# Optimization experiments

Hardware: AMD Instinct MI355X
Metric: run time of the kernel (lower is better)

## Reference

```python
import jax, jax.numpy as jnp
import numpy as np

B, T, D, HS = 8, 2048, 1024, 64


def setup_inputs() -> dict:
    key = jax.random.key(0)
    ks = jax.random.split(key, 7)
    return {
        "x": jax.random.normal(ks[0], (B, T, D), dtype=jnp.float32),
        "Wq": jax.random.normal(ks[1], (D, HS), dtype=jnp.float32) / np.sqrt(D),
        "bq": jax.random.normal(ks[2], (HS,), dtype=jnp.float32) * 0.01,
        "Wk": jax.random.normal(ks[3], (D, HS), dtype=jnp.float32) / np.sqrt(D),
        "bk": jax.random.normal(ks[4], (HS,), dtype=jnp.float32) * 0.01,
        "Wv": jax.random.normal(ks[5], (D, HS), dtype=jnp.float32) / np.sqrt(D),
        "bv": jax.random.normal(ks[6], (HS,), dtype=jnp.float32) * 0.01,
    }


def reference(x, Wq, bq, Wk, bk, Wv, bv):
    # Q,K,V projections: [B,T,D] @ [D,HS] -> [B,T,HS]
    Q = x @ Wq + bq
    K = x @ Wk + bk
    V = x @ Wv + bv
    # raw scores [B,T,T]
    scores = jnp.einsum("bqh,bkh->bqk", Q, K)
    # causal mask applied BEFORE scaling (as in the original; -inf is scale-invariant)
    causal = jnp.tril(jnp.ones((T, T), dtype=bool))
    scores = jnp.where(causal[None, :, :], scores, -jnp.inf)
    scores = scores / jnp.sqrt(jnp.asarray(HS, dtype=scores.dtype))
    attn = jax.nn.softmax(scores, axis=-1)
    # dropout is identity in eval mode (deterministic reference)
    return jnp.einsum("bqk,bkh->bqh", attn, V)
```

## Files before the change

kernel.cpp:

```cpp
#include <hip/hip_runtime.h>
#include <hip/hip_bf16.h>

typedef __bf16 bf16x8 __attribute__((ext_vector_type(8)));
typedef __bf16 bf16x4 __attribute__((ext_vector_type(4)));
typedef float  f32x4  __attribute__((ext_vector_type(4)));

#define B_  8
#define T_  2048
#define D_  1024
#define HS_ 64


__global__ __launch_bounds__(256) void pack_w(
    const float* __restrict__ Wq, const float* __restrict__ Wk,
    const float* __restrict__ Wv, __bf16* __restrict__ Wp)
{
    const int t    = blockIdx.x * 256 + threadIdx.x;
    const int lane = t & 63;
    const int pg   = t >> 6;
    const int s    = pg & 3;
    const int c    = (pg >> 2) & 31;
    const int p    = pg >> 7;
    const int m16  = lane & 15;
    const int quad = lane >> 4;

    const float* W = (p == 0) ? Wq : (p == 1) ? Wk : Wv;
    const float* src = W + (size_t)(c * 32 + quad * 8) * 64 + s * 16 + m16;
    bf16x8 frag;
    #pragma unroll
    for (int j = 0; j < 8; ++j) frag[j] = (__bf16)src[(size_t)j * 64];
    *(bf16x8*)(Wp + (size_t)pg * 512 + lane * 8) = frag;
}

__global__ __launch_bounds__(256) void qkv_fused(
    const float* __restrict__ x,
    const __bf16* __restrict__ Wp,
    const float* __restrict__ bq, const float* __restrict__ bk,
    const float* __restrict__ bv,
    __bf16* __restrict__ Q,
    __bf16* __restrict__ Kp,
    __bf16* __restrict__ Vp)
{
    __shared__ alignas(16) unsigned char Smem[73728];

    const int rt   = blockIdx.x;
    const int wave = threadIdx.x >> 6;
    const int lane = threadIdx.x & 63;
    const int m16  = lane & 15;
    const int quad = lane >> 4;
    const int row0 = rt * 32;

    __bf16* Xs = (__bf16*)(Smem + wave * 16896);

    {
        const float* xsrc = x + (size_t)row0 * 1024 + wave * 256;
        const int sr = lane >> 5;
        const int sc = (lane & 31) * 8;
        #pragma unroll
        for (int i = 0; i < 16; ++i) {
            const int r = i * 2 + sr;
            f32x4 v0 = *(const f32x4*)(xsrc + (size_t)r * 1024 + sc);
            f32x4 v1 = *(const f32x4*)(xsrc + (size_t)r * 1024 + sc + 4);
            bf16x8 w;
            #pragma unroll
            for (int e = 0; e < 4; ++e) { w[e] = (__bf16)v0[e]; w[4 + e] = (__bf16)v1[e]; }
            *(bf16x8*)&Xs[r * 264 + sc] = w;
        }
    }
    __builtin_amdgcn_wave_barrier();

    f32x4 acc[3][4][2];
    #pragma unroll
    for (int p = 0; p < 3; ++p)
        #pragma unroll
        for (int s = 0; s < 4; ++s)
            #pragma unroll
            for (int t = 0; t < 2; ++t) acc[p][s][t] = {0.f, 0.f, 0.f, 0.f};

    bf16x8 bfA[12], bfB[12];

#define WLOAD(BUF, K0)                                                     \
    {                                                                      \
        const int cb_ = wave * 8 + ((K0) >> 5);                            \
        _Pragma("unroll")                                                  \
        for (int ps_ = 0; ps_ < 12; ++ps_) {                               \
            const int p_ = ps_ >> 2, s_ = ps_ & 3;                         \
            BUF[ps_] = *(const bf16x8*)(Wp +                               \
                ((size_t)((p_ * 32 + cb_) * 4 + s_) << 9) + lane * 8);     \
        }                                                                  \
    }
#define KSTEP(BUF, K0)                                                     \
    {                                                                      \
        bf16x8 a0 = *(const bf16x8*)&Xs[m16 * 264 + (K0) + quad * 8];      \
        bf16x8 a1 = *(const bf16x8*)&Xs[(16 + m16) * 264 + (K0) + quad * 8]; \
        __builtin_amdgcn_sched_barrier(0);                                 \
        _Pragma("unroll")                                                  \
        for (int ps_ = 0; ps_ < 12; ++ps_) {                               \
            acc[ps_ >> 2][ps_ & 3][0] =                                    \
                __builtin_amdgcn_mfma_f32_16x16x32_bf16(a0, BUF[ps_], acc[ps_ >> 2][ps_ & 3][0], 0, 0, 0); \
            acc[ps_ >> 2][ps_ & 3][1] =                                    \
                __builtin_amdgcn_mfma_f32_16x16x32_bf16(a1, BUF[ps_], acc[ps_ >> 2][ps_ & 3][1], 0, 0, 0); \
        }                                                                  \
    }

    WLOAD(bfA, 0);
    #pragma unroll
    for (int k0 = 0; k0 < 256; k0 += 64) {
        WLOAD(bfB, k0 + 32);
        KSTEP(bfA, k0);
        if (k0 + 64 < 256) WLOAD(bfA, k0 + 64);
        KSTEP(bfB, k0 + 32);
    }
#undef KSTEP
#undef WLOAD

    f32x4* Red = (f32x4*)Smem;
    __syncthreads();
    if (wave != 0) {
        #pragma unroll
        for (int p = 0; p < 3; ++p)
            #pragma unroll
            for (int s = 0; s < 4; ++s)
                #pragma unroll
                for (int t = 0; t < 2; ++t)
                    Red[((wave - 1) * 24 + (p * 4 + s) * 2 + t) * 64 + lane] = acc[p][s][t];
    }
    __syncthreads();
    if (wave != 0) return;

    #pragma unroll
    for (int p = 0; p < 3; ++p)
        #pragma unroll
        for (int s = 0; s < 4; ++s)
            #pragma unroll
            for (int t = 0; t < 2; ++t) {
                f32x4 sum = acc[p][s][t];
                #pragma unroll
                for (int w = 0; w < 3; ++w) {
                    f32x4 v = Red[(w * 24 + (p * 4 + s) * 2 + t) * 64 + lane];
                    #pragma unroll
                    for (int e = 0; e < 4; ++e) sum[e] += v[e];
                }
                acc[p][s][t] = sum;
            }

    #pragma unroll
    for (int t = 0; t < 2; ++t) {
        const int row0t = row0 + t * 16;

        #pragma unroll
        for (int s = 0; s < 4; ++s) {
            const int h = s * 16 + m16;
            const float bia = bq[h];
            #pragma unroll
            for (int r = 0; r < 4; ++r)
                Q[(size_t)(row0t + quad * 4 + r) * 64 + h] = (__bf16)(acc[0][s][t][r] + bia);
        }

        const int tb = (row0t >> 4) & 3;
        const int jt = (row0t >> 6) & 31;
        const int bb = row0t >> 11;
        __bf16* kpt = Kp + (((size_t)bb * 32 + jt) * 8) * 512;
        __bf16* vpt = Vp + (((size_t)bb * 32 + jt) * 8) * 512;

        {
            const int snb  = ((tb >> 1) << 1) | (quad & 1);
            const int m16b = ((tb & 1) << 3) | ((quad >> 1) << 2);
            #pragma unroll
            for (int s = 0; s < 4; ++s) {
                const int h = s * 16 + m16;
                const float bia = bk[h];
                const int g     = snb * 2 + (s >> 1);
                const int quadc = ((s & 1) << 1) | (m16 >> 3);
                const int j     = m16 & 7;
                #pragma unroll
                for (int r = 0; r < 4; ++r)
                    kpt[(size_t)g * 512 + (quadc * 16 + m16b + r) * 8 + j] =
                        (__bf16)(acc[1][s][t][r] + bia);
            }
        }
        {
            const int lanec = ((((tb & 1) << 1) | (quad >> 1)) << 4) + m16;
            const int jbase = (quad & 1) << 2;
            #pragma unroll
            for (int s = 0; s < 4; ++s) {
                const int h = s * 16 + m16;
                const float bia = bv[h];
                const int g = s * 2 + (tb >> 1);
                bf16x4 pack;
                #pragma unroll
                for (int r = 0; r < 4; ++r) pack[r] = (__bf16)(acc[2][s][t][r] + bia);
                *(bf16x4*)(vpt + (size_t)g * 512 + lanec * 8 + jbase) = pack;
            }
        }
    }
}

__global__ __launch_bounds__(512) void attn_fused(
    const __bf16* __restrict__ Q,
    const __bf16* __restrict__ Kp,
    const __bf16* __restrict__ Vp,
    float* __restrict__ O)
{
    __shared__ float Mrg[8][64][37];

    const int s  = blockIdx.x;
    const int b  = blockIdx.y;
    const int wave = threadIdx.x >> 6;
    const int lane = threadIdx.x & 63;
    const int m16  = lane & 15;
    const int quad = lane >> 4;
    const float SC = 0.18033688f;

    const __bf16* Qb = Q  + (size_t)b * T_ * HS_;
    const __bf16* Kb = Kp + (size_t)b * 32 * 4096;
    const __bf16* Vb = Vp + (size_t)b * 32 * 4096;
    float* Obase     = O  + (size_t)b * T_ * HS_;

    bf16x8 vA[8];

#define LOADK(KA, JT)                                                      \
    {                                                                      \
        const __bf16* kb_ = Kb + (size_t)(JT) * 4096 + lane * 8;           \
        _Pragma("unroll")                                                  \
        for (int g_ = 0; g_ < 8; ++g_) KA[g_] = *(const bf16x8*)(kb_ + g_ * 512); \
    }
#define LOADV(JT)                                                          \
    {                                                                      \
        const __bf16* vb_ = Vb + (size_t)(JT) * 4096 + lane * 8;           \
        _Pragma("unroll")                                                  \
        for (int g_ = 0; g_ < 8; ++g_) vA[g_] = *(const bf16x8*)(vb_ + g_ * 512); \
    }

#define STEP(CK, NK)                                                       \
    {                                                                      \
        const int j0 = jt * 64;                                            \
        LOADV(jt);                       \
        f32x4 svA[4], svB[4];                                              \
        _Pragma("unroll")                                                  \
        for (int sn_ = 0; sn_ < 4; ++sn_) {                                \
            svA[sn_] = {0.f, 0.f, 0.f, 0.f};                               \
            svB[sn_] = {0.f, 0.f, 0.f, 0.f};                               \
            svA[sn_] = __builtin_amdgcn_mfma_f32_16x16x32_bf16(CK[sn_*2],   qA0, svA[sn_], 0, 0, 0); \
            svA[sn_] = __builtin_amdgcn_mfma_f32_16x16x32_bf16(CK[sn_*2+1], qA1, svA[sn_], 0, 0, 0); \
            svB[sn_] = __builtin_amdgcn_mfma_f32_16x16x32_bf16(CK[sn_*2],   qB0, svB[sn_], 0, 0, 0); \
            svB[sn_] = __builtin_amdgcn_mfma_f32_16x16x32_bf16(CK[sn_*2+1], qB1, svB[sn_], 0, 0, 0); \
        }                                                                  \
        if (jt + 8 < ntiles) LOADK(NK, jt + 8);                            \
        __builtin_amdgcn_sched_barrier(0);                                 \
        if (jt == ntiles - 1) {    \
            _Pragma("unroll")                                              \
            for (int sn_ = 0; sn_ < 4; ++sn_) {                            \
                const int kbase = j0 + ((sn_ >> 1) << 5) + (quad << 3) + ((sn_ & 1) << 2); \
                _Pragma("unroll")                                          \
                for (int r_ = 0; r_ < 4; ++r_) {                           \
                    svA[sn_][r_] = (kbase + r_ <= qrowA) ? svA[sn_][r_] : -3e38f; \
                    svB[sn_][r_] = (kbase + r_ <= qrowB) ? svB[sn_][r_] : -3e38f; \
                }                                                          \
            }                                                              \
        }                                                                  \
        float mxA = -3e38f, mxB = -3e38f;                                  \
        _Pragma("unroll")                                                  \
        for (int sn_ = 0; sn_ < 4; ++sn_)                                  \
            _Pragma("unroll")                                              \
            for (int r_ = 0; r_ < 4; ++r_) {                               \
                mxA = fmaxf(mxA, svA[sn_][r_]);                            \
                mxB = fmaxf(mxB, svB[sn_][r_]);                            \
            }                                                              \
        mxA = fmaxf(mxA, __shfl_xor(mxA, 16));                             \
        mxA = fmaxf(mxA, __shfl_xor(mxA, 32));                             \
        mxB = fmaxf(mxB, __shfl_xor(mxB, 16));                             \
        mxB = fmaxf(mxB, __shfl_xor(mxB, 32));                             \
        const float newmA = fmaxf(mA, mxA);                                \
        const float newmB = fmaxf(mB, mxB);                                \
        const float alA = exp2f((mA - newmA) * SC);                        \
        const float alB = exp2f((mB - newmB) * SC);                        \
        mA = newmA; mB = newmB;                                            \
        const float nmA = newmA * SC, nmB = newmB * SC;                    \
        float rsA = 0.f, rsB = 0.f;                                        \
        _Pragma("unroll")                                                  \
        for (int sn_ = 0; sn_ < 4; ++sn_)                                  \
            _Pragma("unroll")                                              \
            for (int r_ = 0; r_ < 4; ++r_) {                               \
                float pa_ = exp2f(__builtin_fmaf(svA[sn_][r_], SC, -nmA)); \
                float pb_ = exp2f(__builtin_fmaf(svB[sn_][r_], SC, -nmB)); \
                svA[sn_][r_] = pa_; rsA += pa_;                            \
                svB[sn_][r_] = pb_; rsB += pb_;                            \
            }                                                              \
        rsA += __shfl_xor(rsA, 16); rsA += __shfl_xor(rsA, 32);            \
        rsB += __shfl_xor(rsB, 16); rsB += __shfl_xor(rsB, 32);            \
        lA = lA * alA + rsA;  lB = lB * alB + rsB;                         \
        _Pragma("unroll")                                                  \
        for (int hs_ = 0; hs_ < 4; ++hs_)                                  \
            _Pragma("unroll")                                              \
            for (int r_ = 0; r_ < 4; ++r_) {                               \
                oA[hs_][r_] *= alA;                                        \
                oB[hs_][r_] *= alB;                                        \
            }                                                              \
        bf16x8 pA0, pA1, pB0, pB1;                                         \
        _Pragma("unroll")                                                  \
        for (int r_ = 0; r_ < 4; ++r_) {                                   \
            pA0[r_]     = (__bf16)svA[0][r_];                              \
            pA0[4 + r_] = (__bf16)svA[1][r_];                              \
            pA1[r_]     = (__bf16)svA[2][r_];                              \
            pA1[4 + r_] = (__bf16)svA[3][r_];                              \
            pB0[r_]     = (__bf16)svB[0][r_];                              \
            pB0[4 + r_] = (__bf16)svB[1][r_];                              \
            pB1[r_]     = (__bf16)svB[2][r_];                              \
            pB1[4 + r_] = (__bf16)svB[3][r_];                              \
        }                                                                  \
        _Pragma("unroll")                                                  \
        for (int hs_ = 0; hs_ < 4; ++hs_) {                                \
            oA[hs_] = __builtin_amdgcn_mfma_f32_16x16x32_bf16(vA[hs_*2],   pA0, oA[hs_], 0, 0, 0); \
            oA[hs_] = __builtin_amdgcn_mfma_f32_16x16x32_bf16(vA[hs_*2+1], pA1, oA[hs_], 0, 0, 0); \
            oB[hs_] = __builtin_amdgcn_mfma_f32_16x16x32_bf16(vA[hs_*2],   pB0, oB[hs_], 0, 0, 0); \
            oB[hs_] = __builtin_amdgcn_mfma_f32_16x16x32_bf16(vA[hs_*2+1], pB1, oB[hs_], 0, 0, 0); \
        }                                                                  \
    }

    auto runPhase = [&](const int f) {
        const int ntiles = (f >> 1) + 1;
        const int qrowA  = f * 32 + m16;
        const int qrowB  = qrowA + 16;

        bf16x8 qA0 = *(const bf16x8*)(Qb + (size_t)qrowA * 64 + quad * 8);
        bf16x8 qA1 = *(const bf16x8*)(Qb + (size_t)qrowA * 64 + 32 + quad * 8);
        bf16x8 qB0 = *(const bf16x8*)(Qb + (size_t)qrowB * 64 + quad * 8);
        bf16x8 qB1 = *(const bf16x8*)(Qb + (size_t)qrowB * 64 + 32 + quad * 8);

        f32x4 oA[4], oB[4];
        #pragma unroll
        for (int hs = 0; hs < 4; ++hs) {
            oA[hs] = {0.f, 0.f, 0.f, 0.f};
            oB[hs] = {0.f, 0.f, 0.f, 0.f};
        }
        float mA = -3e38f, lA = 0.f, mB = -3e38f, lB = 0.f;

        bf16x8 kA[8], kB[8];
        int jt = wave;
        if (jt < ntiles) {
            LOADK(kA, jt);
            while (true) {
                STEP(kA, kB);
                jt += 8; if (jt >= ntiles) break;
                STEP(kB, kA);
                jt += 8; if (jt >= ntiles) break;
            }
        }

        #pragma unroll
        for (int hs = 0; hs < 4; ++hs)
            #pragma unroll
            for (int r = 0; r < 4; ++r) {
                Mrg[wave][lane][hs * 4 + r]      = oA[hs][r];
                Mrg[wave][lane][18 + hs * 4 + r] = oB[hs][r];
            }
        Mrg[wave][lane][16] = mA; Mrg[wave][lane][17] = lA;
        Mrg[wave][lane][34] = mB; Mrg[wave][lane][35] = lB;
        __syncthreads();
        if (wave < 2) {
            const int off  = wave * 18;
            const int qrow = f * 32 + wave * 16 + m16;
            float mw[8], lw[8];
            #pragma unroll
            for (int w = 0; w < 8; ++w) {
                mw[w] = Mrg[w][lane][off + 16];
                lw[w] = Mrg[w][lane][off + 17];
            }
            float M = mw[0];
            #pragma unroll
            for (int w = 1; w < 8; ++w) M = fmaxf(M, mw[w]);
            float aw[8], den = 0.f;
            #pragma unroll
            for (int w = 0; w < 8; ++w) {
                aw[w] = exp2f((mw[w] - M) * SC);
                den += lw[w] * aw[w];
            }
            const float inv = 1.f / den;
            float* Ob = Obase + (size_t)qrow * 64;
            #pragma unroll
            for (int hs = 0; hs < 4; ++hs) {
                f32x4 v;
                #pragma unroll
                for (int r = 0; r < 4; ++r) {
                    float acc = 0.f;
                    #pragma unroll
                    for (int w = 0; w < 8; ++w)
                        acc += Mrg[w][lane][off + hs * 4 + r] * aw[w];
                    v[r] = acc * inv;
                }
                *(f32x4*)(Ob + hs * 16 + quad * 4) = v;
            }
        }
        __syncthreads();
    };

    runPhase(s);
    runPhase(63 - s);
#undef STEP
#undef LOADV
#undef LOADK
}

extern "C" void kernel_launch(void* const* d_in, const int* in_sizes, int n_in,
                              void* d_out, int out_size, void* d_ws, size_t ws_size,
                              hipStream_t stream)
{
    const float* x  = (const float*)d_in[0];
    const float* Wq = (const float*)d_in[1];
    const float* bq = (const float*)d_in[2];
    const float* Wk = (const float*)d_in[3];
    const float* bk = (const float*)d_in[4];
    const float* Wv = (const float*)d_in[5];
    const float* bv = (const float*)d_in[6];
    float* out = (float*)d_out;

    __bf16* Wp = (__bf16*)d_ws;
    __bf16* Q  = Wp + 384 * 512;
    __bf16* Kp = Q  + (size_t)B_ * T_ * HS_;
    __bf16* Vp = Kp + (size_t)B_ * T_ * HS_;

    pack_w<<<96, 256, 0, stream>>>(Wq, Wk, Wv, Wp);
    qkv_fused<<<512, 256, 0, stream>>>(x, Wp, bq, bk, bv, Q, Kp, Vp);
    attn_fused<<<dim3(32, 8), 512, 0, stream>>>(Q, Kp, Vp, out);
}
```

Baseline: 128.1 us.

## Split QKV projection across waves by output tile instead of K-reduction

The QKV projection kernel now processes 16 rows per block (1024 blocks) with a shared 16x1024 bf16 x tile. Each wave owns 3 of the 12 output column tiles and runs the full K=1024 reduction itself, rather than each wave covering a quarter of K and merging partials through LDS. This removes the cross-wave reduction, its LDS traffic and one barrier, shrinks LDS to about 33KB, and cuts accumulator registers so more blocks fit per CU (launch bounds now request 4). In exchange every block rereads the full packed weight matrix, doubling weight traffic from L2, and each wave has a longer serial MFMA chain with fewer independent accumulators.

```diff
diff --git a/kernel.cpp b/kernel.cpp
--- a/kernel.cpp
+++ b/kernel.cpp
@@ -32,7 +32,7 @@
     *(bf16x8*)(Wp + (size_t)pg * 512 + lane * 8) = frag;
 }
 
-__global__ __launch_bounds__(256) void qkv_fused(
+__global__ __launch_bounds__(256, 4) void qkv_fused(
     const float* __restrict__ x,
     const __bf16* __restrict__ Wp,
     const float* __restrict__ bq, const float* __restrict__ bk,
@@ -41,157 +41,109 @@
     __bf16* __restrict__ Kp,
     __bf16* __restrict__ Vp)
 {
-    __shared__ alignas(16) unsigned char Smem[73728];
+    __shared__ alignas(16) __bf16 Xs[16 * 1032];
 
     const int rt   = blockIdx.x;
     const int wave = threadIdx.x >> 6;
     const int lane = threadIdx.x & 63;
     const int m16  = lane & 15;
     const int quad = lane >> 4;
-    const int row0 = rt * 32;
-
-    __bf16* Xs = (__bf16*)(Smem + wave * 16896);
+    const int row0 = rt * 16;
 
     {
         const float* xsrc = x + (size_t)row0 * 1024 + wave * 256;
         const int sr = lane >> 5;
         const int sc = (lane & 31) * 8;
         #pragma unroll
-        for (int i = 0; i < 16; ++i) {
+        for (int i = 0; i < 8; ++i) {
             const int r = i * 2 + sr;
             f32x4 v0 = *(const f32x4*)(xsrc + (size_t)r * 1024 + sc);
             f32x4 v1 = *(const f32x4*)(xsrc + (size_t)r * 1024 + sc + 4);
             bf16x8 w;
             #pragma unroll
             for (int e = 0; e < 4; ++e) { w[e] = (__bf16)v0[e]; w[4 + e] = (__bf16)v1[e]; }
-            *(bf16x8*)&Xs[r * 264 + sc] = w;
-        }
-    }
-    __builtin_amdgcn_wave_barrier();
-
-    f32x4 acc[3][4][2];
-    #pragma unroll
-    for (int p = 0; p < 3; ++p)
-        #pragma unroll
-        for (int s = 0; s < 4; ++s)
-            #pragma unroll
-            for (int t = 0; t < 2; ++t) acc[p][s][t] = {0.f, 0.f, 0.f, 0.f};
-
-    bf16x8 bfA[12], bfB[12];
-
-#define WLOAD(BUF, K0)                                                     \
-    {                                                                      \
-        const int cb_ = wave * 8 + ((K0) >> 5);                            \
-        _Pragma("unroll")                                                  \
-        for (int ps_ = 0; ps_ < 12; ++ps_) {                               \
-            const int p_ = ps_ >> 2, s_ = ps_ & 3;                         \
-            BUF[ps_] = *(const bf16x8*)(Wp +                               \
-                ((size_t)((p_ * 32 + cb_) * 4 + s_) << 9) + lane * 8);     \
-        }                                                                  \
-    }
-#define KSTEP(BUF, K0)                                                     \
-    {                                                                      \
-        bf16x8 a0 = *(const bf16x8*)&Xs[m16 * 264 + (K0) + quad * 8];      \
-        bf16x8 a1 = *(const bf16x8*)&Xs[(16 + m16) * 264 + (K0) + quad * 8]; \
+            *(bf16x8*)&Xs[r * 1032 + wave * 256 + sc] = w;
+        }
+    }
+    __syncthreads();
+
+    const int ps0 = wave * 3;
+    const __bf16* wb[3];
+    #pragma unroll
+    for (int j = 0; j < 3; ++j) {
+        const int ps = ps0 + j, p = ps >> 2, s = ps & 3;
+        wb[j] = Wp + (size_t)p * 65536 + s * 512 + lane * 8;
+    }
+    const __bf16* ab = &Xs[m16 * 1032 + quad * 8];
+
+    f32x4 acc[3];
+    #pragma unroll
+    for (int j = 0; j < 3; ++j) acc[j] = {0.f, 0.f, 0.f, 0.f};
+
+    bf16x8 bfA[3], bfB[3];
+
+#define WLOAD(BUF, C)                                                      \
+    {                                                                      \
+        _Pragma("unroll")                                                  \
+        for (int j_ = 0; j_ < 3; ++j_)                                     \
+            BUF[j_] = *(const bf16x8*)(wb[j_] + (size_t)(C) * 2048);       \
+    }
+#define KSTEP(BUF, C)                                                      \
+    {                                                                      \
+        bf16x8 a_ = *(const bf16x8*)(ab + (C) * 32);                       \
         __builtin_amdgcn_sched_barrier(0);                                 \
         _Pragma("unroll")                                                  \
-        for (int ps_ = 0; ps_ < 12; ++ps_) {                               \
-            acc[ps_ >> 2][ps_ & 3][0] =                                    \
-                __builtin_amdgcn_mfma_f32_16x16x32_bf16(a0, BUF[ps_], acc[ps_ >> 2][ps_ & 3][0], 0, 0, 0); \
-            acc[ps_ >> 2][ps_ & 3][1] =                                    \
-                __builtin_amdgcn_mfma_f32_16x16x32_bf16(a1, BUF[ps_], acc[ps_ >> 2][ps_ & 3][1], 0, 0, 0); \
-        }                                                                  \
+        for (int j_ = 0; j_ < 3; ++j_)                                     \
+            acc[j_] = __builtin_amdgcn_mfma_f32_16x16x32_bf16(a_, BUF[j_], acc[j_], 0, 0, 0); \
     }
 
     WLOAD(bfA, 0);
-    #pragma unroll
-    for (int k0 = 0; k0 < 256; k0 += 64) {
-        WLOAD(bfB, k0 + 32);
-        KSTEP(bfA, k0);
-        if (k0 + 64 < 256) WLOAD(bfA, k0 + 64);
-        KSTEP(bfB, k0 + 32);
+    WLOAD(bfB, 1);
+    #pragma unroll
+    for (int c = 0; c < 32; c += 2) {
+        KSTEP(bfA, c);
+        if (c + 2 < 32) WLOAD(bfA, c + 2);
+        KSTEP(bfB, c + 1);
+        if (c + 3 < 32) WLOAD(bfB, c + 3);
     }
 #undef KSTEP
 #undef WLOAD
 
-    f32x4* Red = (f32x4*)Smem;
-    __syncthreads();
-    if (wave != 0) {
-        #pragma unroll
-        for (int p = 0; p < 3; ++p)
-            #pragma unroll
-            for (int s = 0; s < 4; ++s)
-                #pragma unroll
-                for (int t = 0; t < 2; ++t)
-                    Red[((wave - 1) * 24 + (p * 4 + s) * 2 + t) * 64 + lane] = acc[p][s][t];
-    }
-    __syncthreads();
-    if (wave != 0) return;
-
-    #pragma unroll
-    for (int p = 0; p < 3; ++p)
-        #pragma unroll
-        for (int s = 0; s < 4; ++s)
-            #pragma unroll
-            for (int t = 0; t < 2; ++t) {
-                f32x4 sum = acc[p][s][t];
-                #pragma unroll
-                for (int w = 0; w < 3; ++w) {
-                    f32x4 v = Red[(w * 24 + (p * 4 + s) * 2 + t) * 64 + lane];
-                    #pragma unroll
-                    for (int e = 0; e < 4; ++e) sum[e] += v[e];
-                }
-                acc[p][s][t] = sum;
-            }
-
-    #pragma unroll
-    for (int t = 0; t < 2; ++t) {
-        const int row0t = row0 + t * 16;
-
-        #pragma unroll
-        for (int s = 0; s < 4; ++s) {
-            const int h = s * 16 + m16;
+    const int tb = (row0 >> 4) & 3;
+    const int jt = (row0 >> 6) & 31;
+    const int bb = row0 >> 11;
+
+    #pragma unroll
+    for (int j = 0; j < 3; ++j) {
+        const int ps = ps0 + j, p = ps >> 2, s = ps & 3;
+        const int h = s * 16 + m16;
+        if (p == 0) {
             const float bia = bq[h];
             #pragma unroll
             for (int r = 0; r < 4; ++r)
-                Q[(size_t)(row0t + quad * 4 + r) * 64 + h] = (__bf16)(acc[0][s][t][r] + bia);
-        }
-
-        const int tb = (row0t >> 4) & 3;
-        const int jt = (row0t >> 6) & 31;
-        const int bb = row0t >> 11;
-        __bf16* kpt = Kp + (((size_t)bb * 32 + jt) * 8) * 512;
-        __bf16* vpt = Vp + (((size_t)bb * 32 + jt) * 8) * 512;
-
-        {
-            const int snb  = ((tb >> 1) << 1) | (quad & 1);
-            const int m16b = ((tb & 1) << 3) | ((quad >> 1) << 2);
-            #pragma unroll
-            for (int s = 0; s < 4; ++s) {
-                const int h = s * 16 + m16;
-                const float bia = bk[h];
-                const int g     = snb * 2 + (s >> 1);
-                const int quadc = ((s & 1) << 1) | (m16 >> 3);
-                const int j     = m16 & 7;
-                #pragma unroll
-                for (int r = 0; r < 4; ++r)
-                    kpt[(size_t)g * 512 + (quadc * 16 + m16b + r) * 8 + j] =
-                        (__bf16)(acc[1][s][t][r] + bia);
-            }
-        }
-        {
+                Q[(size_t)(row0 + quad * 4 + r) * 64 + h] = (__bf16)(acc[j][r] + bia);
+        } else if (p == 1) {
+            __bf16* kpt = Kp + (((size_t)bb * 32 + jt) * 8) * 512;
+            const int snb   = ((tb >> 1) << 1) | (quad & 1);
+            const int m16b  = ((tb & 1) << 3) | ((quad >> 1) << 2);
+            const int g     = snb * 2 + (s >> 1);
+            const int quadc = ((s & 1) << 1) | (m16 >> 3);
+            const int jj    = m16 & 7;
+            const float bia = bk[h];
+            #pragma unroll
+            for (int r = 0; r < 4; ++r)
+                kpt[(size_t)g * 512 + (quadc * 16 + m16b + r) * 8 + jj] =
+                    (__bf16)(acc[j][r] + bia);
+        } else {
+            __bf16* vpt = Vp + (((size_t)bb * 32 + jt) * 8) * 512;
             const int lanec = ((((tb & 1) << 1) | (quad >> 1)) << 4) + m16;
             const int jbase = (quad & 1) << 2;
-            #pragma unroll
-            for (int s = 0; s < 4; ++s) {
-                const int h = s * 16 + m16;
-                const float bia = bv[h];
-                const int g = s * 2 + (tb >> 1);
-                bf16x4 pack;
-                #pragma unroll
-                for (int r = 0; r < 4; ++r) pack[r] = (__bf16)(acc[2][s][t][r] + bia);
-                *(bf16x4*)(vpt + (size_t)g * 512 + lanec * 8 + jbase) = pack;
-            }
+            const int g     = s * 2 + (tb >> 1);
+            const float bia = bv[h];
+            bf16x4 pack;
+            #pragma unroll
+            for (int r = 0; r < 4; ++r) pack[r] = (__bf16)(acc[j][r] + bia);
+            *(bf16x4*)(vpt + (size_t)g * 512 + lanec * 8 + jbase) = pack;
         }
     }
 }
@@ -421,6 +373,6 @@
     __bf16* Vp = Kp + (size_t)B_ * T_ * HS_;
 
     pack_w<<<96, 256, 0, stream>>>(Wq, Wk, Wv, Wp);
-    qkv_fused<<<512, 256, 0, stream>>>(x, Wp, bq, bk, bv, Q, Kp, Vp);
+    qkv_fused<<<1024, 256, 0, stream>>>(x, Wp, bq, bk, bv, Q, Kp, Vp);
     attn_fused<<<dim3(32, 8), 512, 0, stream>>>(Q, Kp, Vp, out);
 }
```

New measurement: 132.2 us. 1.03x slower.

## Stream x chunks through a triple-buffered LDS ring overlapped with MFMA

Applied to the files above, without the earlier changes.

The QKV projection kernel no longer loads each wave's full 32x256 x slice into LDS before computing. It now streams 32-column chunks through a 3-slot per-wave LDS ring, issuing the global load for the next chunk before the current chunk's MFMAs and writing it after them. This is meant to hide the global x load latency behind compute and to cut per-wave LDS use. In exchange the schedule is more intricate, and correctness relies on intra-wave ordering with no explicit barriers between the ring writes and reads.

```diff
diff --git a/kernel.cpp b/kernel.cpp
--- a/kernel.cpp
+++ b/kernel.cpp
@@ -50,24 +50,29 @@
     const int quad = lane >> 4;
     const int row0 = rt * 32;
 
-    __bf16* Xs = (__bf16*)(Smem + wave * 16896);
-
-    {
-        const float* xsrc = x + (size_t)row0 * 1024 + wave * 256;
-        const int sr = lane >> 5;
-        const int sc = (lane & 31) * 8;
-        #pragma unroll
-        for (int i = 0; i < 16; ++i) {
-            const int r = i * 2 + sr;
-            f32x4 v0 = *(const f32x4*)(xsrc + (size_t)r * 1024 + sc);
-            f32x4 v1 = *(const f32x4*)(xsrc + (size_t)r * 1024 + sc + 4);
-            bf16x8 w;
-            #pragma unroll
-            for (int e = 0; e < 4; ++e) { w[e] = (__bf16)v0[e]; w[4 + e] = (__bf16)v1[e]; }
-            *(bf16x8*)&Xs[r * 264 + sc] = w;
-        }
-    }
-    __builtin_amdgcn_wave_barrier();
+    __bf16* Xc = (__bf16*)(Smem + wave * 7680);
+    const int srow = lane >> 3;
+    const int scol = (lane & 7) * 4;
+    const float* xbase = x + (size_t)row0 * 1024 + wave * 256;
+
+#define XLOAD(REGS, C)                                                     \
+    {                                                                      \
+        const float* xp_ = xbase + (C) * 32 + scol;                        \
+        _Pragma("unroll")                                                  \
+        for (int i_ = 0; i_ < 4; ++i_)                                     \
+            REGS[i_] = *(const f32x4*)(xp_ + (size_t)(srow + 8 * i_) * 1024); \
+    }
+#define XWRITE(REGS, C)                                                    \
+    {                                                                      \
+        __bf16* xs_ = Xc + ((C) % 3) * 1280 + srow * 40 + scol;            \
+        _Pragma("unroll")                                                  \
+        for (int i_ = 0; i_ < 4; ++i_) {                                   \
+            bf16x4 w_;                                                     \
+            _Pragma("unroll")                                              \
+            for (int e_ = 0; e_ < 4; ++e_) w_[e_] = (__bf16)REGS[i_][e_];  \
+            *(bf16x4*)(xs_ + 8 * i_ * 40) = w_;                            \
+        }                                                                  \
+    }
 
     f32x4 acc[3][4][2];
     #pragma unroll
@@ -78,10 +83,11 @@
             for (int t = 0; t < 2; ++t) acc[p][s][t] = {0.f, 0.f, 0.f, 0.f};
 
     bf16x8 bfA[12], bfB[12];
-
-#define WLOAD(BUF, K0)                                                     \
-    {                                                                      \
-        const int cb_ = wave * 8 + ((K0) >> 5);                            \
+    f32x4 xr[4];
+
+#define WLOAD(BUF, C)                                                      \
+    {                                                                      \
+        const int cb_ = wave * 8 + (C);                                    \
         _Pragma("unroll")                                                  \
         for (int ps_ = 0; ps_ < 12; ++ps_) {                               \
             const int p_ = ps_ >> 2, s_ = ps_ & 3;                         \
@@ -89,10 +95,10 @@
                 ((size_t)((p_ * 32 + cb_) * 4 + s_) << 9) + lane * 8);     \
         }                                                                  \
     }
-#define KSTEP(BUF, K0)                                                     \
-    {                                                                      \
-        bf16x8 a0 = *(const bf16x8*)&Xs[m16 * 264 + (K0) + quad * 8];      \
-        bf16x8 a1 = *(const bf16x8*)&Xs[(16 + m16) * 264 + (K0) + quad * 8]; \
+#define KSTEP(BUF, C)                                                      \
+    {                                                                      \
+        bf16x8 a0 = *(const bf16x8*)&Xc[((C) % 3) * 1280 + m16 * 40 + quad * 8]; \
+        bf16x8 a1 = *(const bf16x8*)&Xc[((C) % 3) * 1280 + (16 + m16) * 40 + quad * 8]; \
         __builtin_amdgcn_sched_barrier(0);                                 \
         _Pragma("unroll")                                                  \
         for (int ps_ = 0; ps_ < 12; ++ps_) {                               \
@@ -103,16 +109,30 @@
         }                                                                  \
     }
 
+    XLOAD(xr, 0);  XWRITE(xr, 0);
+    XLOAD(xr, 1);  XWRITE(xr, 1);
     WLOAD(bfA, 0);
-    #pragma unroll
-    for (int k0 = 0; k0 < 256; k0 += 64) {
-        WLOAD(bfB, k0 + 32);
-        KSTEP(bfA, k0);
-        if (k0 + 64 < 256) WLOAD(bfA, k0 + 64);
-        KSTEP(bfB, k0 + 32);
-    }
+    WLOAD(bfB, 1);
+    __builtin_amdgcn_wave_barrier();
+
+    XLOAD(xr, 2);
+    KSTEP(bfA, 0);  XWRITE(xr, 2);  WLOAD(bfA, 2);
+    XLOAD(xr, 3);
+    KSTEP(bfB, 1);  XWRITE(xr, 3);  WLOAD(bfB, 3);
+    XLOAD(xr, 4);
+    KSTEP(bfA, 2);  XWRITE(xr, 4);  WLOAD(bfA, 4);
+    XLOAD(xr, 5);
+    KSTEP(bfB, 3);  XWRITE(xr, 5);  WLOAD(bfB, 5);
+    XLOAD(xr, 6);
+    KSTEP(bfA, 4);  XWRITE(xr, 6);  WLOAD(bfA, 6);
+    XLOAD(xr, 7);
+    KSTEP(bfB, 5);  XWRITE(xr, 7);  WLOAD(bfB, 7);
+    KSTEP(bfA, 6);
+    KSTEP(bfB, 7);
 #undef KSTEP
 #undef WLOAD
+#undef XWRITE
+#undef XLOAD
 
     f32x4* Red = (f32x4*)Smem;
     __syncthreads();
```

After: 133.9 us. +4.6%, slower.
